# Optimization experiments

Hardware: AMD Instinct MI355X
Metric: run time of the kernel (lower is better)

## Reference

```python
import jax, jax.numpy as jnp
import numpy as np

N = 500_000      # total observations
D = 40           # per-observation feature dim
S = 2048         # number of segments (time series)
WIDTH = 128      # psi hidden width
LATENT = 128     # latent width
DOT = 64         # dot_prod_dim
HEADS = 4        # n_heads


def setup_inputs() -> dict:
    key = jax.random.key(0)
    ks = jax.random.split(key, 12)

    def he(k, shape):
        fan_in = shape[0]
        lim = np.sqrt(6.0 / fan_in)
        return jax.random.uniform(k, shape, jnp.float32, -lim, lim)

    inputs = jax.random.normal(ks[0], (N, D), jnp.float32)
    segment_ids = jnp.sort(jax.random.randint(ks[1], (N,), 0, S))
    lengths = jax.random.randint(ks[2], (S,), 0, 300)
    return {
        "inputs": inputs,
        "segment_ids": segment_ids,
        "lengths": lengths,
        "W1": he(ks[3], (D, WIDTH)),      "b1": jnp.zeros((WIDTH,), jnp.float32),
        "W2": he(ks[4], (WIDTH, WIDTH)), "b2": jnp.zeros((WIDTH,), jnp.float32),
        "W3": he(ks[5], (WIDTH, LATENT)),"b3": jnp.zeros((LATENT,), jnp.float32),
        "Wr": he(ks[6], (LATENT, LATENT)),"br": jnp.zeros((LATENT,), jnp.float32),
        "W_k": he(ks[7], (LATENT + D, DOT * HEADS)),
        "W_q": jax.random.normal(ks[8], (HEADS, DOT), jnp.float32) * 0.02,
    }


def segment_softmax(x, seg, num_segments):
    # x: [N, H]; softmax over elements sharing the same segment id
    m = jax.ops.segment_max(x, seg, num_segments, indices_are_sorted=True)
    e = jnp.exp(x - m[seg])
    denom = jax.ops.segment_sum(e, seg, num_segments, indices_are_sorted=True)
    return e / denom[seg]


def reference(inputs, segment_ids, lengths, W1, b1, W2, b2, W3, b3, Wr, br, W_k, W_q):
    relu = jax.nn.relu
    # psi: 2 hidden dense layers + latent projection (all relu)
    h = relu(inputs @ W1 + b1)
    h = relu(h @ W2 + b2)
    enc = relu(h @ W3 + b3)                                   # [N, LATENT]
    # segment mean aggregation
    sums = jax.ops.segment_sum(enc, segment_ids, S, indices_are_sorted=True)
    counts = jax.ops.segment_sum(jnp.ones((enc.shape[0], 1), enc.dtype),
                                 segment_ids, S, indices_are_sorted=True)
    agg = sums / jnp.maximum(counts, 1.0)                      # [S, LATENT]
    agg = relu(agg @ Wr + br)                                  # rho
    # broadcast back and combine
    combined = jnp.concatenate([inputs, agg[segment_ids]], axis=-1)  # [N, D+LATENT]
    keys = (combined @ W_k).reshape(-1, HEADS, DOT)            # split+stack == reshape
    preattn = jnp.einsum('nhd,hd->nh', keys, W_q) / jnp.sqrt(jnp.float32(DOT))
    attn = segment_softmax(preattn, segment_ids, S)            # [N, H]
    # match original: list of per-head [N, 1] tensors -> stacked [H, N, 1]
    return jnp.transpose(attn)[..., None]
```

## Files before the change

### kernel.cpp

```cpp
#include <hip/hip_runtime.h>
#include <math.h>


#define NROWS 500000
#define DIM 40
#define NQ (DIM / 4)
#define NSEG 2048
#define DOTD 64
#define NH 4
#define ABLOCK 256
#define CROWS 512

__global__ __launch_bounds__(ABLOCK) void fused_logits_kernel(
    const float* __restrict__ x,
    const int* __restrict__ seg,
    const float* __restrict__ Wk,
    const float* __restrict__ Wq,
    int* __restrict__ seg_start,
    int* __restrict__ seg_end,
    float4* __restrict__ logit4)
{
    __shared__ __align__(16) float wxl[NH][DIM];

    const int tid = (int)threadIdx.x;

    if (tid < DIM * NH) {
        const int h = tid & 3;
        const int d = tid >> 2;
        const float4* wkp = (const float4*)(Wk + d * (NH * DOTD) + h * DOTD);
        const float4* wqp = (const float4*)(Wq + h * DOTD);
        float acc = 0.f;
        #pragma unroll
        for (int j = 0; j < DOTD / 4; ++j) {
            const float4 a = wkp[j];
            const float4 b = wqp[j];
            acc += a.x * b.x + a.y * b.y + a.z * b.z + a.w * b.w;
        }
        wxl[h][d] = acc * 0.125f;
    }
    __syncthreads();

    const int n = (int)(blockIdx.x * ABLOCK + tid);
    if (n >= NROWS) return;

    const int s = seg[n];
    if (n == 0) {
        seg_start[s] = 0;
        for (int t = 0; t < s; ++t) { seg_start[t] = 0; seg_end[t] = 0; }
    } else {
        const int sp = seg[n - 1];
        if (sp != s) {
            seg_start[s] = n;
            seg_end[sp] = n;
            for (int t = sp + 1; t < s; ++t) { seg_start[t] = n; seg_end[t] = n; }
        }
    }
    if (n == NROWS - 1) {
        seg_end[s] = NROWS;
        for (int t = s + 1; t < NSEG; ++t) { seg_start[t] = NROWS; seg_end[t] = NROWS; }
    }

    const float4* xr = (const float4*)(x + (size_t)n * DIM);
    float a[NH] = {0.f, 0.f, 0.f, 0.f};
    #pragma unroll
    for (int q = 0; q < NQ; ++q) {
        const float4 v = xr[q];
        #pragma unroll
        for (int h = 0; h < NH; ++h) {
            const float4 w = ((const float4*)wxl[h])[q];
            a[h] += v.x * w.x + v.y * w.y + v.z * w.z + v.w * w.w;
        }
    }
    logit4[n] = make_float4(a[0], a[1], a[2], a[3]);
}

__global__ __launch_bounds__(64) void seg_softmax_kernel(
    const float4* __restrict__ logit4,
    const int* __restrict__ seg_start,
    const int* __restrict__ seg_end,
    float* __restrict__ out)
{
    __shared__ __align__(16) float4 cache4[CROWS];

    const int lane = (int)threadIdx.x;
    const int s = (int)blockIdx.x;
    const int start = seg_start[s];
    const int rows = seg_end[s] - start;
    if (rows <= 0) return;

    float ml[NH], sl[NH];
    #pragma unroll
    for (int h = 0; h < NH; ++h) { ml[h] = -3.0e38f; sl[h] = 0.f; }

    for (int i = lane; i < rows; i += 64) {
        const float4 l4 = logit4[start + i];
        if (i < CROWS) cache4[i] = l4;
        const float l[NH] = {l4.x, l4.y, l4.z, l4.w};
        #pragma unroll
        for (int h = 0; h < NH; ++h) {
            const float nm = fmaxf(ml[h], l[h]);
            sl[h] = sl[h] * __expf(ml[h] - nm) + __expf(l[h] - nm);
            ml[h] = nm;
        }
    }

    float m[NH], rden[NH];
    #pragma unroll
    for (int h = 0; h < NH; ++h) {
        float M = ml[h];
        #pragma unroll
        for (int off = 32; off > 0; off >>= 1) M = fmaxf(M, __shfl_xor(M, off, 64));
        float S = sl[h] * __expf(ml[h] - M);
        #pragma unroll
        for (int off = 32; off > 0; off >>= 1) S += __shfl_xor(S, off, 64);
        m[h] = M;
        rden[h] = 1.0f / S;
    }

    for (int i = lane; i < rows; i += 64) {
        const float4 l4 = (i < CROWS) ? cache4[i] : logit4[start + i];
        const float l[NH] = {l4.x, l4.y, l4.z, l4.w};
        const int n = start + i;
        #pragma unroll
        for (int h = 0; h < NH; ++h)
            out[(size_t)h * NROWS + n] = __expf(l[h] - m[h]) * rden[h];
    }
}

extern "C" void kernel_launch(void* const* d_in, const int* in_sizes, int n_in,
                              void* d_out, int out_size, void* d_ws, size_t ws_size,
                              hipStream_t stream) {
    const float* x  = (const float*)d_in[0];
    const int* seg  = (const int*)d_in[1];
    const float* Wk = (const float*)d_in[11];
    const float* Wq = (const float*)d_in[12];
    float* out = (float*)d_out;

    int* seg_start = (int*)d_ws;
    int* seg_end   = seg_start + NSEG;
    float4* logit4 = (float4*)((char*)d_ws + 16384);

    const int nblk = (NROWS + ABLOCK - 1) / ABLOCK;
    hipLaunchKernelGGL(fused_logits_kernel, dim3(nblk), dim3(ABLOCK),
                       0, stream, x, seg, Wk, Wq, seg_start, seg_end, logit4);
    hipLaunchKernelGGL(seg_softmax_kernel, dim3(NSEG), dim3(64),
                       0, stream, logit4, seg_start, seg_end, out);
}
```

Baseline: 163.1 us.

## Coalesce input loads via padded LDS staging and widen segment softmax blocks

The logits kernel now stages each block's 256 input rows into padded shared memory through fully coalesced float4 loads, rather than having each thread read its own strided 160-byte row. The segment softmax moves from one 64-thread wave per segment to a 256-thread block. It holds up to 512 logits in registers and replaces the online max/sum with a two-pass max-then-sum using cross-wave shared-memory reductions. The goal is better global-memory coalescing and more parallelism per segment, at the cost of extra LDS use (about 45KB per block, which limits occupancy) and extra syncs.

```diff
diff --git a/kernel.cpp b/kernel.cpp
--- a/kernel.cpp
+++ b/kernel.cpp
@@ -9,7 +9,8 @@
 #define DOTD 64
 #define NH 4
 #define ABLOCK 256
-#define CROWS 512
+#define ROWSPB 256
+#define PADW 44
 
 __global__ __launch_bounds__(ABLOCK) void fused_logits_kernel(
     const float* __restrict__ x,
@@ -20,9 +21,26 @@
     int* __restrict__ seg_end,
     float4* __restrict__ logit4)
 {
+    __shared__ __align__(16) float xs[ROWSPB * PADW];
     __shared__ __align__(16) float wxl[NH][DIM];
 
     const int tid = (int)threadIdx.x;
+    const int base = (int)blockIdx.x * ROWSPB;
+    const float4* x4 = (const float4*)x;
+
+    const int g0 = base * NQ;
+    const int gend = NROWS * NQ;
+    #pragma unroll
+    for (int it = 0; it < NQ; ++it) {
+        const int g = g0 + it * ABLOCK + tid;
+        if (g < gend) {
+            const float4 v = x4[g];
+            const int loc = it * ABLOCK + tid;
+            const int r = loc / NQ;
+            const int q = loc - r * NQ;
+            *(float4*)&xs[r * PADW + q * 4] = v;
+        }
+    }
 
     if (tid < DIM * NH) {
         const int h = tid & 3;
@@ -40,7 +58,7 @@
     }
     __syncthreads();
 
-    const int n = (int)(blockIdx.x * ABLOCK + tid);
+    const int n = base + tid;
     if (n >= NROWS) return;
 
     const int s = seg[n];
@@ -60,11 +78,10 @@
         for (int t = s + 1; t < NSEG; ++t) { seg_start[t] = NROWS; seg_end[t] = NROWS; }
     }
 
-    const float4* xr = (const float4*)(x + (size_t)n * DIM);
     float a[NH] = {0.f, 0.f, 0.f, 0.f};
     #pragma unroll
     for (int q = 0; q < NQ; ++q) {
-        const float4 v = xr[q];
+        const float4 v = *(const float4*)&xs[tid * PADW + q * 4];
         #pragma unroll
         for (int h = 0; h < NH; ++h) {
             const float4 w = ((const float4*)wxl[h])[q];
@@ -74,56 +91,94 @@
     logit4[n] = make_float4(a[0], a[1], a[2], a[3]);
 }
 
-__global__ __launch_bounds__(64) void seg_softmax_kernel(
+__global__ __launch_bounds__(ABLOCK) void seg_softmax_kernel(
     const float4* __restrict__ logit4,
     const int* __restrict__ seg_start,
     const int* __restrict__ seg_end,
     float* __restrict__ out)
 {
-    __shared__ __align__(16) float4 cache4[CROWS];
-
-    const int lane = (int)threadIdx.x;
+    __shared__ float redm[4][NH];
+    __shared__ float reds[4][NH];
+
+    const int tid = (int)threadIdx.x;
     const int s = (int)blockIdx.x;
     const int start = seg_start[s];
     const int rows = seg_end[s] - start;
     if (rows <= 0) return;
 
-    float ml[NH], sl[NH];
-    #pragma unroll
-    for (int h = 0; h < NH; ++h) { ml[h] = -3.0e38f; sl[h] = 0.f; }
-
-    for (int i = lane; i < rows; i += 64) {
-        const float4 l4 = logit4[start + i];
-        if (i < CROWS) cache4[i] = l4;
-        const float l[NH] = {l4.x, l4.y, l4.z, l4.w};
-        #pragma unroll
-        for (int h = 0; h < NH; ++h) {
-            const float nm = fmaxf(ml[h], l[h]);
-            sl[h] = sl[h] * __expf(ml[h] - nm) + __expf(l[h] - nm);
-            ml[h] = nm;
-        }
-    }
-
-    float m[NH], rden[NH];
+    const int lane = tid & 63;
+    const int wid = tid >> 6;
+    const float4 NEG = make_float4(-3.0e38f, -3.0e38f, -3.0e38f, -3.0e38f);
+
+    const int i0 = tid, i1 = tid + 256;
+    const float4 la = (i0 < rows) ? logit4[start + i0] : NEG;
+    const float4 lb = (i1 < rows) ? logit4[start + i1] : NEG;
+
+    float lmax[NH] = {fmaxf(la.x, lb.x), fmaxf(la.y, lb.y),
+                      fmaxf(la.z, lb.z), fmaxf(la.w, lb.w)};
+    for (int i = tid + 512; i < rows; i += ABLOCK) {
+        const float4 t = logit4[start + i];
+        lmax[0] = fmaxf(lmax[0], t.x); lmax[1] = fmaxf(lmax[1], t.y);
+        lmax[2] = fmaxf(lmax[2], t.z); lmax[3] = fmaxf(lmax[3], t.w);
+    }
     #pragma unroll
     for (int h = 0; h < NH; ++h) {
-        float M = ml[h];
-        #pragma unroll
-        for (int off = 32; off > 0; off >>= 1) M = fmaxf(M, __shfl_xor(M, off, 64));
-        float S = sl[h] * __expf(ml[h] - M);
-        #pragma unroll
-        for (int off = 32; off > 0; off >>= 1) S += __shfl_xor(S, off, 64);
-        m[h] = M;
-        rden[h] = 1.0f / S;
-    }
-
-    for (int i = lane; i < rows; i += 64) {
-        const float4 l4 = (i < CROWS) ? cache4[i] : logit4[start + i];
-        const float l[NH] = {l4.x, l4.y, l4.z, l4.w};
+        float v = lmax[h];
+        #pragma unroll
+        for (int off = 32; off > 0; off >>= 1) v = fmaxf(v, __shfl_xor(v, off, 64));
+        if (lane == 0) redm[wid][h] = v;
+    }
+    __syncthreads();
+    float m[NH];
+    #pragma unroll
+    for (int h = 0; h < NH; ++h)
+        m[h] = fmaxf(fmaxf(redm[0][h], redm[1][h]),
+                     fmaxf(redm[2][h], redm[3][h]));
+
+    float lsum[NH] = {
+        __expf(la.x - m[0]) + __expf(lb.x - m[0]),
+        __expf(la.y - m[1]) + __expf(lb.y - m[1]),
+        __expf(la.z - m[2]) + __expf(lb.z - m[2]),
+        __expf(la.w - m[3]) + __expf(lb.w - m[3])};
+    for (int i = tid + 512; i < rows; i += ABLOCK) {
+        const float4 t = logit4[start + i];
+        lsum[0] += __expf(t.x - m[0]); lsum[1] += __expf(t.y - m[1]);
+        lsum[2] += __expf(t.z - m[2]); lsum[3] += __expf(t.w - m[3]);
+    }
+    #pragma unroll
+    for (int h = 0; h < NH; ++h) {
+        float v = lsum[h];
+        #pragma unroll
+        for (int off = 32; off > 0; off >>= 1) v += __shfl_xor(v, off, 64);
+        if (lane == 0) reds[wid][h] = v;
+    }
+    __syncthreads();
+    float rden[NH];
+    #pragma unroll
+    for (int h = 0; h < NH; ++h)
+        rden[h] = 1.0f / (reds[0][h] + reds[1][h] + reds[2][h] + reds[3][h]);
+
+    if (i0 < rows) {
+        const int n = start + i0;
+        out[(size_t)0 * NROWS + n] = __expf(la.x - m[0]) * rden[0];
+        out[(size_t)1 * NROWS + n] = __expf(la.y - m[1]) * rden[1];
+        out[(size_t)2 * NROWS + n] = __expf(la.z - m[2]) * rden[2];
+        out[(size_t)3 * NROWS + n] = __expf(la.w - m[3]) * rden[3];
+    }
+    if (i1 < rows) {
+        const int n = start + i1;
+        out[(size_t)0 * NROWS + n] = __expf(lb.x - m[0]) * rden[0];
+        out[(size_t)1 * NROWS + n] = __expf(lb.y - m[1]) * rden[1];
+        out[(size_t)2 * NROWS + n] = __expf(lb.z - m[2]) * rden[2];
+        out[(size_t)3 * NROWS + n] = __expf(lb.w - m[3]) * rden[3];
+    }
+    for (int i = tid + 512; i < rows; i += ABLOCK) {
+        const float4 t = logit4[start + i];
         const int n = start + i;
-        #pragma unroll
-        for (int h = 0; h < NH; ++h)
-            out[(size_t)h * NROWS + n] = __expf(l[h] - m[h]) * rden[h];
+        out[(size_t)0 * NROWS + n] = __expf(t.x - m[0]) * rden[0];
+        out[(size_t)1 * NROWS + n] = __expf(t.y - m[1]) * rden[1];
+        out[(size_t)2 * NROWS + n] = __expf(t.z - m[2]) * rden[2];
+        out[(size_t)3 * NROWS + n] = __expf(t.w - m[3]) * rden[3];
     }
 }
 
@@ -140,9 +195,9 @@
     int* seg_end   = seg_start + NSEG;
     float4* logit4 = (float4*)((char*)d_ws + 16384);
 
-    const int nblk = (NROWS + ABLOCK - 1) / ABLOCK;
+    const int nblk = (NROWS + ROWSPB - 1) / ROWSPB;
     hipLaunchKernelGGL(fused_logits_kernel, dim3(nblk), dim3(ABLOCK),
                        0, stream, x, seg, Wk, Wq, seg_start, seg_end, logit4);
-    hipLaunchKernelGGL(seg_softmax_kernel, dim3(NSEG), dim3(64),
+    hipLaunchKernelGGL(seg_softmax_kernel, dim3(NSEG), dim3(ABLOCK),
                        0, stream, logit4, seg_start, seg_end, out);
 }
```

Measured after the change: 171.7 us. 5.3% more time.
